# Optimization experiments

Measured on AMD Instinct MI355X. Metric: run time of the kernel, lower is better.

The kernel has to match this reference:

```python
import jax, jax.numpy as jnp
import numpy as np

B, Q, D, H, P, F = 16, 300, 256, 8, 4, 2048
HG = WG = 100          # feature-map height/width (hw = 10000, perfect square)
HW = HG * WG
DH = D // H
EPS = 1e-5


def _ln(x, g, b):
    m = x.mean(-1, keepdims=True)
    v = jnp.var(x, axis=-1, keepdims=True)
    return (x - m) * jax.lax.rsqrt(v + EPS) * g + b


def setup_inputs() -> dict:
    key = jax.random.key(0)
    ks = jax.random.split(key, 24)
    rn = lambda k, shape, s=0.02: jax.random.normal(k, shape, jnp.float32) * s
    return {
        "tgt": jax.random.normal(ks[0], (B, Q, D), jnp.float32),
        "memory": jax.random.normal(ks[1], (B, HW, D), jnp.float32),
        "in_proj_w": rn(ks[2], (D, 3 * D)), "in_proj_b": rn(ks[3], (3 * D,)),
        "out_proj_w": rn(ks[4], (D, D)), "out_proj_b": rn(ks[5], (D,)),
        "norm1_g": jnp.ones((D,), jnp.float32), "norm1_b": jnp.zeros((D,), jnp.float32),
        "ref_w": rn(ks[6], (D, 2)), "ref_b": rn(ks[7], (2,)),
        "off_w": rn(ks[8], (D, H * P * 2)), "off_b": rn(ks[9], (H * P * 2,)),
        "attw_w": rn(ks[10], (D, H * P)), "attw_b": rn(ks[11], (H * P,)),
        "vproj_w": rn(ks[12], (D, D)), "vproj_b": rn(ks[13], (D,)),
        "oproj_w": rn(ks[14], (D, D)), "oproj_b": rn(ks[15], (D,)),
        "norm2_g": jnp.ones((D,), jnp.float32), "norm2_b": jnp.zeros((D,), jnp.float32),
        "lin1_w": rn(ks[16], (D, F)), "lin1_b": rn(ks[17], (F,)),
        "lin2_w": rn(ks[18], (F, D)), "lin2_b": rn(ks[19], (D,)),
        "norm3_g": jnp.ones((D,), jnp.float32), "norm3_b": jnp.zeros((D,), jnp.float32),
    }


def reference(tgt, memory, in_proj_w, in_proj_b, out_proj_w, out_proj_b,
              norm1_g, norm1_b, ref_w, ref_b, off_w, off_b, attw_w, attw_b,
              vproj_w, vproj_b, oproj_w, oproj_b, norm2_g, norm2_b,
              lin1_w, lin1_b, lin2_w, lin2_b, norm3_g, norm3_b):
    # ---- self-attention (nn.MultiheadAttention, eval mode: dropout = identity)
    qkv = tgt @ in_proj_w + in_proj_b                      # [B,Q,3D]
    q, k, v = jnp.split(qkv, 3, axis=-1)
    q = q.reshape(B, Q, H, DH)
    k = k.reshape(B, Q, H, DH)
    v = v.reshape(B, Q, H, DH)
    scores = jnp.einsum('bqhd,bkhd->bhqk', q, k) / jnp.sqrt(jnp.float32(DH))
    attn = jax.nn.softmax(scores, axis=-1)
    sa = jnp.einsum('bhqk,bkhd->bqhd', attn, v).reshape(B, Q, D) @ out_proj_w + out_proj_b
    x = _ln(tgt + sa, norm1_g, norm1_b)

    # ---- reference points
    ref = jax.nn.sigmoid(x @ ref_w + ref_b)                # [B,Q,2] in (0,1)

    # ---- deformable cross-attention
    offs = (x @ off_w + off_b).reshape(B, Q, H, P, 2)
    wts = jax.nn.softmax((x @ attw_w + attw_b).reshape(B, Q, H, P), axis=-1)
    vals = (memory @ vproj_w + vproj_b).reshape(B, HW, H, DH)
    loc = jnp.clip(ref[:, :, None, None, :] + offs, 0.0, 1.0)
    sx = loc[..., 0] * (WG - 1)
    sy = loc[..., 1] * (HG - 1)
    x0 = jnp.floor(sx)
    y0 = jnp.floor(sy)
    x0i = jnp.clip(x0.astype(jnp.int32), 0, WG - 1)
    y0i = jnp.clip(y0.astype(jnp.int32), 0, HG - 1)
    x1i = jnp.clip(x0i + 1, 0, WG - 1)
    y1i = jnp.clip(y0i + 1, 0, HG - 1)
    wx1 = sx - x0
    wx0 = 1.0 - wx1
    wy1 = sy - y0
    wy0 = 1.0 - wy1
    bi = jnp.arange(B)[:, None, None, None]
    hi = jnp.arange(H)[None, None, :, None]

    def gather(yi, xi):                                    # [B,Q,H,P,DH]
        return vals[bi, yi * WG + xi, hi]

    samp = (gather(y0i, x0i) * (wx0 * wy0)[..., None]
            + gather(y1i, x0i) * (wx0 * wy1)[..., None]
            + gather(y0i, x1i) * (wx1 * wy0)[..., None]
            + gather(y1i, x1i) * (wx1 * wy1)[..., None])
    ca = (samp * wts[..., None]).sum(axis=3).reshape(B, Q, D) @ oproj_w + oproj_b
    x = _ln(x + ca, norm2_g, norm2_b)

    # ---- FFN
    ff = jax.nn.relu(x @ lin1_w + lin1_b) @ lin2_w + lin2_b
    return _ln(x + ff, norm3_g, norm3_b)
```

## Files before the change

### kernel.cpp

```cpp
#include <hip/hip_runtime.h>

#define NB   16
#define NQ   300
#define ND   256
#define NH   8
#define NP   4
#define NF   2048
#define NHW  10000
#define NWG  100
#define NROW 4800

typedef __attribute__((ext_vector_type(8))) short bf16x8;
typedef __attribute__((ext_vector_type(4))) float f32x4;

__device__ __forceinline__ unsigned short f2bf(float f) {
    unsigned u = __builtin_bit_cast(unsigned, f);
    u = (u + 0x7fffu + ((u >> 16) & 1u)) >> 16;
    return (unsigned short)u;
}
__device__ __forceinline__ float bf2f(unsigned short h) {
    unsigned u = ((unsigned)h) << 16;
    return __builtin_bit_cast(float, u);
}

__global__ __launch_bounds__(256) void transpose_cast(
    const float* __restrict__ w_in,  const float* __restrict__ w_out,
    const float* __restrict__ w_vp,  const float* __restrict__ w_op,
    const float* __restrict__ w_l1,  const float* __restrict__ w_l2,
    unsigned short* __restrict__ o_in, unsigned short* __restrict__ o_out,
    unsigned short* __restrict__ o_vp, unsigned short* __restrict__ o_op,
    unsigned short* __restrict__ o_l1, unsigned short* __restrict__ o_l2)
{
    __shared__ float ts[64][65];
    int b = blockIdx.x;
    const float* src; unsigned short* dst; int K, N, ncx;
    if      (b < 48)  { src = w_in;  dst = o_in;  K = 256;  N = 768;  ncx = 12; }
    else if (b < 64)  { src = w_out; dst = o_out; K = 256;  N = 256;  ncx = 4;  b -= 48; }
    else if (b < 80)  { src = w_vp;  dst = o_vp;  K = 256;  N = 256;  ncx = 4;  b -= 64; }
    else if (b < 96)  { src = w_op;  dst = o_op;  K = 256;  N = 256;  ncx = 4;  b -= 80; }
    else if (b < 224) { src = w_l1;  dst = o_l1;  K = 256;  N = 2048; ncx = 32; b -= 96; }
    else              { src = w_l2;  dst = o_l2;  K = 2048; N = 256;  ncx = 4;  b -= 224; }
    const int n0 = (b % ncx) * 64, k0 = (b / ncx) * 64;
    const int t = threadIdx.x;
    const int r = t >> 4, c = t & 15;
    #pragma unroll
    for (int j = 0; j < 4; j++) {
        float4 v = *(const float4*)(src + (long)(k0 + j * 16 + r) * N + n0 + c * 4);
        ts[j * 16 + r][c * 4 + 0] = v.x;
        ts[j * 16 + r][c * 4 + 1] = v.y;
        ts[j * 16 + r][c * 4 + 2] = v.z;
        ts[j * 16 + r][c * 4 + 3] = v.w;
    }
    __syncthreads();
    #pragma unroll
    for (int j = 0; j < 4; j++) {
        unsigned short o[4];
        #pragma unroll
        for (int i = 0; i < 4; i++)
            o[i] = f2bf(ts[c * 4 + i][j * 16 + r]);
        *(uint2*)(dst + (long)(n0 + j * 16 + r) * K + k0 + c * 4) = *(uint2*)o;
    }
}

__global__ __launch_bounds__(256) void prep_head(
    const float* __restrict__ rw, const float* __restrict__ rb,
    const float* __restrict__ ow, const float* __restrict__ ob,
    const float* __restrict__ aw, const float* __restrict__ ab,
    unsigned short* __restrict__ o_hd, float* __restrict__ o_hb)
{
    int id = blockIdx.x * 256 + threadIdx.x;
    if (id < 32768) {
        int n = id >> 8, k = id & 255;
        float v;
        if (n < 2)       v = rw[k * 2 + n];
        else if (n < 66) v = ow[k * 64 + (n - 2)];
        else if (n < 98) v = aw[k * 32 + (n - 66)];
        else             v = 0.0f;
        o_hd[id] = f2bf(v);
        return;
    }
    id -= 32768;
    if (id < 128) {
        float v;
        if (id < 2)       v = rb[id];
        else if (id < 66) v = ob[id - 2];
        else if (id < 98) v = ab[id - 66];
        else              v = 0.0f;
        o_hb[id] = v;
    }
}

template <int RELU, int OUTBF, int SPLITK, int TM>
__global__ __launch_bounds__(256, (TM == 64) ? 4 : 3) void gemm_bt(
    const float* __restrict__ A, const unsigned short* __restrict__ Bt,
    const float* __restrict__ bias, void* __restrict__ Cout,
    int M, int N, int K)
{
    constexpr int AI = TM / 32;
    constexpr int NI = TM / 32;
    __shared__ unsigned short As[2][TM][40];
    __shared__ unsigned short Bs[2][128][40];
    const int t    = threadIdx.x;
    const long m0  = (long)blockIdx.y * TM;
    const int  n0  = blockIdx.x * 128;
    const int  wave = t >> 6, lane = t & 63;
    const int  wm  = (wave >> 1) * (TM / 2);
    const int  wn  = (wave & 1) << 6;
    const int  l16 = lane & 15, quad = lane >> 4;
    const int  arow = t >> 3, acol = (t & 7) << 2;
    const int  brow = t >> 2, bcol = (t & 3) << 3;

    f32x4 acc[NI][4] = {};

    const int kChunk = K / SPLITK;
    const int kBeg   = (SPLITK > 1) ? blockIdx.z * kChunk : 0;
    const int nk     = kChunk / 32;

    float4 fa[AI];
    uint4  fb[2];

    auto loadAB = [&](int kt) {
        const int k0 = kBeg + kt * 32;
        #pragma unroll
        for (int j = 0; j < AI; j++) {
            const long r = m0 + j * 32 + arow;
            fa[j] = (r < M) ? *(const float4*)(A + r * (long)K + k0 + acol)
                            : make_float4(0.f, 0.f, 0.f, 0.f);
        }
        #pragma unroll
        for (int j = 0; j < 2; j++)
            fb[j] = *(const uint4*)(Bt + (long)(n0 + j * 64 + brow) * K + k0 + bcol);
    };
    auto storeLDS = [&](int buf) {
        #pragma unroll
        for (int j = 0; j < AI; j++) {
            unsigned short ta[4] = {f2bf(fa[j].x), f2bf(fa[j].y),
                                    f2bf(fa[j].z), f2bf(fa[j].w)};
            *(uint2*)&As[buf][j * 32 + arow][acol] = *(uint2*)ta;
        }
        #pragma unroll
        for (int j = 0; j < 2; j++)
            *(uint4*)&Bs[buf][j * 64 + brow][bcol] = fb[j];
    };

    loadAB(0);
    storeLDS(0);
    __syncthreads();

    for (int kt = 0; kt < nk; kt++) {
        const int cur = kt & 1;
        if (kt + 1 < nk) loadAB(kt + 1);

        bf16x8 af[NI], bfr[4];
        #pragma unroll
        for (int i = 0; i < NI; i++)
            af[i] = *(const bf16x8*)&As[cur][wm + i * 16 + l16][quad * 8];
        #pragma unroll
        for (int j = 0; j < 4; j++)
            bfr[j] = *(const bf16x8*)&Bs[cur][wn + j * 16 + l16][quad * 8];
        #pragma unroll
        for (int i = 0; i < NI; i++)
            #pragma unroll
            for (int j = 0; j < 4; j++)
                acc[i][j] = __builtin_amdgcn_mfma_f32_16x16x32_bf16(
                    bfr[j], af[i], acc[i][j], 0, 0, 0);

        if (kt + 1 < nk) {
            storeLDS(cur ^ 1);
            __syncthreads();
        }
    }

    float4 bj[4];
    #pragma unroll
    for (int j = 0; j < 4; j++)
        bj[j] = *(const float4*)&bias[n0 + wn + j * 16 + quad * 4];

    if (SPLITK > 1) {
        const float bscale = (blockIdx.z == 0) ? 1.0f : 0.0f;
        #pragma unroll
        for (int i = 0; i < NI; i++) {
            const long gr = m0 + wm + i * 16 + l16;
            if (gr < M) {
                #pragma unroll
                for (int j = 0; j < 4; j++) {
                    float* cp = (float*)Cout + gr * N + n0 + wn + j * 16 + quad * 4;
                    atomicAdd(cp + 0, acc[i][j][0] + bscale * bj[j].x);
                    atomicAdd(cp + 1, acc[i][j][1] + bscale * bj[j].y);
                    atomicAdd(cp + 2, acc[i][j][2] + bscale * bj[j].z);
                    atomicAdd(cp + 3, acc[i][j][3] + bscale * bj[j].w);
                }
            }
        }
        return;
    }

    #pragma unroll
    for (int i = 0; i < NI; i++) {
        const long gr = m0 + wm + i * 16 + l16;
        if (gr < M) {
            #pragma unroll
            for (int j = 0; j < 4; j++) {
                float4 v;
                v.x = acc[i][j][0] + bj[j].x;
                v.y = acc[i][j][1] + bj[j].y;
                v.z = acc[i][j][2] + bj[j].z;
                v.w = acc[i][j][3] + bj[j].w;
                if (RELU) {
                    v.x = fmaxf(v.x, 0.f); v.y = fmaxf(v.y, 0.f);
                    v.z = fmaxf(v.z, 0.f); v.w = fmaxf(v.w, 0.f);
                }
                const int gc = n0 + wn + j * 16 + quad * 4;
                if (OUTBF) {
                    unsigned short o[4] = {f2bf(v.x), f2bf(v.y), f2bf(v.z), f2bf(v.w)};
                    *(uint2*)((unsigned short*)Cout + gr * N + gc) = *(uint2*)o;
                } else {
                    *(float4*)((float*)Cout + gr * N + gc) = v;
                }
            }
        }
    }
}

__global__ __launch_bounds__(256) void attn_kernel(
    const float* __restrict__ qkv, float* __restrict__ sa)
{
    __shared__ union {
        struct {
            unsigned short Ks[304][40];
            unsigned short Qs[64][40];
        } s;
        unsigned short Ps[4][16][328];
    } u;
    __shared__ unsigned short Vt[32][328];

    const int bh = blockIdx.y;
    const int b  = bh >> 3, h = bh & 7;
    const int q0 = blockIdx.x * 64;
    const int t  = threadIdx.x;

    for (int idx = t; idx < 304 * 8; idx += 256) {
        const int r = idx >> 3, c4 = (idx & 7) << 2;
        if (r < NQ) {
            const float4 kv = *(const float4*)(qkv + ((long)(b * NQ + r)) * 768 + 256 + h * 32 + c4);
            u.s.Ks[r][c4 + 0] = f2bf(kv.x); u.s.Ks[r][c4 + 1] = f2bf(kv.y);
            u.s.Ks[r][c4 + 2] = f2bf(kv.z); u.s.Ks[r][c4 + 3] = f2bf(kv.w);
        } else {
            u.s.Ks[r][c4 + 0] = 0; u.s.Ks[r][c4 + 1] = 0;
            u.s.Ks[r][c4 + 2] = 0; u.s.Ks[r][c4 + 3] = 0;
        }
    }
    for (int idx = t; idx < NQ * 8; idx += 256) {
        const int key = idx >> 3, dq = (idx & 7) << 2;
        const float4 vv = *(const float4*)(qkv + ((long)(b * NQ + key)) * 768 + 512 + h * 32 + dq);
        Vt[dq + 0][key] = f2bf(vv.x); Vt[dq + 1][key] = f2bf(vv.y);
        Vt[dq + 2][key] = f2bf(vv.z); Vt[dq + 3][key] = f2bf(vv.w);
    }
    for (int idx = t; idx < 32 * 20; idx += 256)
        Vt[idx / 20][300 + idx % 20] = 0;
    for (int idx = t; idx < 64 * 8; idx += 256) {
        const int r = idx >> 3, c4 = (idx & 7) << 2;
        const int q = q0 + r;
        if (q < NQ) {
            const float4 qv = *(const float4*)(qkv + ((long)(b * NQ + q)) * 768 + h * 32 + c4);
            u.s.Qs[r][c4 + 0] = f2bf(qv.x); u.s.Qs[r][c4 + 1] = f2bf(qv.y);
            u.s.Qs[r][c4 + 2] = f2bf(qv.z); u.s.Qs[r][c4 + 3] = f2bf(qv.w);
        } else {
            u.s.Qs[r][c4 + 0] = 0; u.s.Qs[r][c4 + 1] = 0;
            u.s.Qs[r][c4 + 2] = 0; u.s.Qs[r][c4 + 3] = 0;
        }
    }
    __syncthreads();

    const int wave = t >> 6, lane = t & 63;
    const int l16 = lane & 15, quad = lane >> 4;
    const float scale = 0.1767766952966369f;

    const bf16x8 aq = *(const bf16x8*)&u.s.Qs[wave * 16 + l16][quad * 8];
    f32x4 sacc[19];
    #pragma unroll
    for (int kt = 0; kt < 19; kt++) {
        const bf16x8 bk = *(const bf16x8*)&u.s.Ks[kt * 16 + l16][quad * 8];
        sacc[kt] = __builtin_amdgcn_mfma_f32_16x16x32_bf16(
            aq, bk, (f32x4){0.f, 0.f, 0.f, 0.f}, 0, 0, 0);
    }

    float inv[4];
    #pragma unroll
    for (int r = 0; r < 4; r++) {
        float m = -1e30f;
        #pragma unroll
        for (int kt = 0; kt < 19; kt++) {
            float s = sacc[kt][r] * scale;
            if (kt == 18 && l16 >= 12) s = -1e30f;
            sacc[kt][r] = s;
            m = fmaxf(m, s);
        }
        m = fmaxf(m, __shfl_xor(m, 1)); m = fmaxf(m, __shfl_xor(m, 2));
        m = fmaxf(m, __shfl_xor(m, 4)); m = fmaxf(m, __shfl_xor(m, 8));
        float sum = 0.f;
        #pragma unroll
        for (int kt = 0; kt < 19; kt++) {
            float p = __expf(sacc[kt][r] - m);
            sacc[kt][r] = p;
            sum += p;
        }
        sum += __shfl_xor(sum, 1); sum += __shfl_xor(sum, 2);
        sum += __shfl_xor(sum, 4); sum += __shfl_xor(sum, 8);
        inv[r] = 1.0f / sum;
    }

    __syncthreads();

    #pragma unroll
    for (int kt = 0; kt < 19; kt++)
        #pragma unroll
        for (int r = 0; r < 4; r++)
            u.Ps[wave][quad * 4 + r][kt * 16 + l16] = f2bf(sacc[kt][r] * inv[r]);
    #pragma unroll
    for (int r = 0; r < 4; r++)
        u.Ps[wave][quad * 4 + r][304 + l16] = 0;

    f32x4 o0 = {0.f, 0.f, 0.f, 0.f}, o1 = {0.f, 0.f, 0.f, 0.f};
    #pragma unroll
    for (int kt = 0; kt < 10; kt++) {
        const bf16x8 ap  = *(const bf16x8*)&u.Ps[wave][l16][kt * 32 + quad * 8];
        const bf16x8 bv0 = *(const bf16x8*)&Vt[l16][kt * 32 + quad * 8];
        const bf16x8 bv1 = *(const bf16x8*)&Vt[16 + l16][kt * 32 + quad * 8];
        o0 = __builtin_amdgcn_mfma_f32_16x16x32_bf16(ap, bv0, o0, 0, 0, 0);
        o1 = __builtin_amdgcn_mfma_f32_16x16x32_bf16(ap, bv1, o1, 0, 0, 0);
    }

    #pragma unroll
    for (int r = 0; r < 4; r++) {
        const int q = q0 + wave * 16 + quad * 4 + r;
        if (q < NQ) {
            float* op = sa + ((long)(b * NQ + q)) * ND + h * 32;
            op[l16]      = o0[r];
            op[16 + l16] = o1[r];
        }
    }
}

__global__ __launch_bounds__(256) void residual_ln(
    const float* __restrict__ a, const float* __restrict__ r,
    const float* __restrict__ gam, const float* __restrict__ bet,
    float* __restrict__ out)
{
    const int row  = blockIdx.x * 4 + (threadIdx.x >> 6);
    const int lane = threadIdx.x & 63;
    const long base = (long)row * ND + lane * 4;
    float4 av = *(const float4*)(a + base);
    float4 rv = *(const float4*)(r + base);
    float x0 = av.x + rv.x, x1 = av.y + rv.y, x2 = av.z + rv.z, x3 = av.w + rv.w;
    float s  = x0 + x1 + x2 + x3;
    float s2 = x0 * x0 + x1 * x1 + x2 * x2 + x3 * x3;
    #pragma unroll
    for (int off = 32; off >= 1; off >>= 1) {
        s  += __shfl_xor(s, off);
        s2 += __shfl_xor(s2, off);
    }
    float mean = s * 0.00390625f;
    float var  = s2 * 0.00390625f - mean * mean;
    float rstd = rsqrtf(var + 1e-5f);
    float4 gv = *(const float4*)(gam + lane * 4);
    float4 bv = *(const float4*)(bet + lane * 4);
    float4 o;
    o.x = (x0 - mean) * rstd * gv.x + bv.x;
    o.y = (x1 - mean) * rstd * gv.y + bv.y;
    o.z = (x2 - mean) * rstd * gv.z + bv.z;
    o.w = (x3 - mean) * rstd * gv.w + bv.w;
    *(float4*)(out + base) = o;
}

__global__ __launch_bounds__(256) void meta_kernel(
    const float* __restrict__ res, float* __restrict__ meta)
{
    const int t   = threadIdx.x;
    const int row = blockIdx.x * 8 + (t >> 5);
    const int s   = t & 31;
    const int h   = s >> 2;
    const float* rp = res + (long)row * 128;
    const float rx = 1.f / (1.f + __expf(-rp[0]));
    const float ry = 1.f / (1.f + __expf(-rp[1]));
    const float offx = rp[2 + 2 * s], offy = rp[3 + 2 * s];
    const float a0 = rp[66 + h * 4 + 0], a1 = rp[66 + h * 4 + 1];
    const float a2 = rp[66 + h * 4 + 2], a3 = rp[66 + h * 4 + 3];
    const float mx = fmaxf(fmaxf(a0, a1), fmaxf(a2, a3));
    const float den = __expf(a0 - mx) + __expf(a1 - mx) +
                      __expf(a2 - mx) + __expf(a3 - mx);
    const float awt = __expf(rp[66 + s] - mx) / den;

    const float lx = fminf(fmaxf(rx + offx, 0.f), 1.f) * (NWG - 1);
    const float ly = fminf(fmaxf(ry + offy, 0.f), 1.f) * (NWG - 1);
    const float fx = floorf(lx), fy = floorf(ly);
    int x0 = (int)fx; x0 = min(max(x0, 0), NWG - 1);
    int y0 = (int)fy; y0 = min(max(y0, 0), NWG - 1);
    const int x1 = min(x0 + 1, NWG - 1);
    const int y1 = min(y0 + 1, NWG - 1);
    const float wx1 = lx - fx, wx0 = 1.f - wx1;
    const float wy1 = ly - fy, wy0 = 1.f - wy1;
    float4 m0, m1;
    m0.x = __int_as_float(y0 * NWG + x0);
    m0.y = __int_as_float(y0 * NWG + x1);
    m0.z = __int_as_float(y1 * NWG + x0);
    m0.w = __int_as_float(y1 * NWG + x1);
    m1.x = awt * wx0 * wy0;
    m1.y = awt * wx1 * wy0;
    m1.z = awt * wx0 * wy1;
    m1.w = awt * wx1 * wy1;
    float* mp = meta + (long)row * 256 + s * 8;
    *(float4*)mp       = m0;
    *(float4*)(mp + 4) = m1;
}

__global__ __launch_bounds__(256) void deform_gather(
    const float* __restrict__ meta, const unsigned short* __restrict__ vals,
    float* __restrict__ ca)
{
    const int row = blockIdx.x;
    const int b = row / NQ;
    __shared__ float ms[256];
    const int t = threadIdx.x;
    ms[t] = meta[(long)row * 256 + t];
    __syncthreads();
    const int h = t >> 5, d = t & 31;
    const unsigned short* vb = vals + (long)b * NHW * ND + h * 32 + d;
    float acc = 0.f;
    #pragma unroll
    for (int p = 0; p < NP; p++) {
        const float* mp = ms + h * 32 + p * 8;
        const int i00 = __float_as_int(mp[0]);
        const int i01 = __float_as_int(mp[1]);
        const int i10 = __float_as_int(mp[2]);
        const int i11 = __float_as_int(mp[3]);
        acc += mp[4] * bf2f(vb[(long)i00 * ND]);
        acc += mp[5] * bf2f(vb[(long)i01 * ND]);
        acc += mp[6] * bf2f(vb[(long)i10 * ND]);
        acc += mp[7] * bf2f(vb[(long)i11 * ND]);
    }
    ca[(long)row * ND + t] = acc;
}

extern "C" void kernel_launch(void* const* d_in, const int* in_sizes, int n_in,
                              void* d_out, int out_size, void* d_ws, size_t ws_size,
                              hipStream_t stream)
{
    (void)in_sizes; (void)n_in; (void)out_size; (void)ws_size;
    const float* tgt   = (const float*)d_in[0];
    const float* mem   = (const float*)d_in[1];
    const float* inpw  = (const float*)d_in[2];
    const float* inpb  = (const float*)d_in[3];
    const float* outw  = (const float*)d_in[4];
    const float* outb  = (const float*)d_in[5];
    const float* n1g   = (const float*)d_in[6];
    const float* n1b   = (const float*)d_in[7];
    const float* refw  = (const float*)d_in[8];
    const float* refb  = (const float*)d_in[9];
    const float* offw  = (const float*)d_in[10];
    const float* offb  = (const float*)d_in[11];
    const float* attww = (const float*)d_in[12];
    const float* attwb = (const float*)d_in[13];
    const float* vpw   = (const float*)d_in[14];
    const float* vpb   = (const float*)d_in[15];
    const float* opw   = (const float*)d_in[16];
    const float* opb   = (const float*)d_in[17];
    const float* n2g   = (const float*)d_in[18];
    const float* n2b   = (const float*)d_in[19];
    const float* l1w   = (const float*)d_in[20];
    const float* l1b   = (const float*)d_in[21];
    const float* l2w   = (const float*)d_in[22];
    const float* l2b   = (const float*)d_in[23];
    const float* n3g   = (const float*)d_in[24];
    const float* n3b   = (const float*)d_in[25];
    float* out = (float*)d_out;

    char* p = (char*)d_ws;
    auto alloc = [&](size_t bytes) {
        char* r = p; p += (bytes + 255) & ~(size_t)255; return (void*)r;
    };
    unsigned short* wtIn   = (unsigned short*)alloc(768 * 256 * 2);
    unsigned short* wtOut  = (unsigned short*)alloc(256 * 256 * 2);
    unsigned short* wtVp   = (unsigned short*)alloc(256 * 256 * 2);
    unsigned short* wtOp   = (unsigned short*)alloc(256 * 256 * 2);
    unsigned short* wtL1   = (unsigned short*)alloc(2048 * 256 * 2);
    unsigned short* wtL2   = (unsigned short*)alloc(256 * 2048 * 2);
    unsigned short* wtHead = (unsigned short*)alloc(128 * 256 * 2);
    float*          headb  = (float*)alloc(128 * 4);
    float* qkv  = (float*)alloc((size_t)NROW * 768 * 4);
    float* sa   = (float*)alloc((size_t)NROW * ND * 4);
    float* x1   = (float*)alloc((size_t)NROW * ND * 4);
    float* x2   = (float*)alloc((size_t)NROW * ND * 4);
    float* tmp  = (float*)alloc((size_t)NROW * ND * 4);
    float* ca   = (float*)alloc((size_t)NROW * ND * 4);
    float* meta = (float*)alloc((size_t)NROW * 256 * 4);
    void* uni = alloc((size_t)NB * NHW * ND * 2);
    unsigned short* vals = (unsigned short*)uni;
    float* h1 = (float*)uni;
    float* res = qkv;

    transpose_cast<<<352, 256, 0, stream>>>(
        inpw, outw, vpw, opw, l1w, l2w,
        wtIn, wtOut, wtVp, wtOp, wtL1, wtL2);
    prep_head<<<129, 256, 0, stream>>>(refw, refb, offw, offb, attww, attwb,
                                       wtHead, headb);

    gemm_bt<0, 0, 1, 64><<<dim3(6, 75), 256, 0, stream>>>(tgt, wtIn, inpb, qkv,
                                                          NROW, 768, 256);
    gemm_bt<0, 1, 1, 128><<<dim3(2, 1250), 256, 0, stream>>>(mem, wtVp, vpb, vals,
                                                             NB * NHW, 256, 256);
    attn_kernel<<<dim3(5, 128), 256, 0, stream>>>(qkv, sa);
    gemm_bt<0, 0, 1, 64><<<dim3(2, 75), 256, 0, stream>>>(sa, wtOut, outb, tmp,
                                                          NROW, 256, 256);
    residual_ln<<<1200, 256, 0, stream>>>(tgt, tmp, n1g, n1b, x1);
    gemm_bt<0, 0, 1, 64><<<dim3(1, 75), 256, 0, stream>>>(x1, wtHead, headb, res,
                                                          NROW, 128, 256);
    meta_kernel<<<600, 256, 0, stream>>>(res, meta);
    deform_gather<<<4800, 256, 0, stream>>>(meta, vals, ca);
    gemm_bt<0, 0, 1, 64><<<dim3(2, 75), 256, 0, stream>>>(ca, wtOp, opb, tmp,
                                                          NROW, 256, 256);
    residual_ln<<<1200, 256, 0, stream>>>(x1, tmp, n2g, n2b, x2);
    gemm_bt<1, 0, 1, 64><<<dim3(16, 75), 256, 0, stream>>>(x2, wtL1, l1b, h1,
                                                           NROW, 2048, 256);
    hipMemsetAsync(tmp, 0, (size_t)NROW * ND * 4, stream);
    gemm_bt<0, 0, 4, 64><<<dim3(2, 75, 4), 256, 0, stream>>>(h1, wtL2, l2b, tmp,
                                                             NROW, 256, 2048);
    residual_ln<<<1200, 256, 0, stream>>>(x2, tmp, n3g, n3b, out);
}
```

Baseline: 577.1 us.

## Add full-width vproj GEMM and replace split-K atomics with partial-sum buffers

Adds a dedicated value-projection GEMM in which each block computes a 128x256 output tile, so every A tile of the large memory tensor is loaded and converted to bf16 once instead of twice. The split-K FFN second GEMM now writes each K-slice to its own partial buffer instead of using atomicAdd, and the memset is dropped. The final residual LayerNorm sums the four partials before normalizing. The costs are extra workspace, larger accumulator register use (launch bound of 2 blocks per CU), and three more partial-tensor reads in the last LayerNorm.

After: 516.5 us. 1.12x faster.

```diff
diff --git a/kernel.cpp b/kernel.cpp
--- a/kernel.cpp
+++ b/kernel.cpp
@@ -87,6 +87,93 @@
         else if (id < 98) v = ab[id - 66];
         else              v = 0.0f;
         o_hb[id] = v;
+    }
+}
+
+__global__ __launch_bounds__(256, 2) void gemm_vproj(
+    const float* __restrict__ A, const unsigned short* __restrict__ Bt,
+    const float* __restrict__ bias, unsigned short* __restrict__ Cout)
+{
+    __shared__ unsigned short As[2][128][40];
+    __shared__ unsigned short Bs[2][256][40];
+    const int t    = threadIdx.x;
+    const long m0  = (long)blockIdx.x * 128;
+    const int  wave = t >> 6, lane = t & 63;
+    const int  wm  = (wave >> 1) << 6;
+    const int  wn  = (wave & 1) << 7;
+    const int  l16 = lane & 15, quad = lane >> 4;
+    const int  arow = t >> 3, acol = (t & 7) << 2;
+    const int  brow = t >> 2, bcol = (t & 3) << 3;
+
+    f32x4 acc[4][8] = {};
+    float4 fa[4];
+    uint4  fb[4];
+
+    auto loadAB = [&](int k0) {
+        #pragma unroll
+        for (int j = 0; j < 4; j++)
+            fa[j] = *(const float4*)(A + (m0 + j * 32 + arow) * 256L + k0 + acol);
+        #pragma unroll
+        for (int j = 0; j < 4; j++)
+            fb[j] = *(const uint4*)(Bt + (j * 64 + brow) * 256L + k0 + bcol);
+    };
+    auto storeLDS = [&](int buf) {
+        #pragma unroll
+        for (int j = 0; j < 4; j++) {
+            unsigned short ta[4] = {f2bf(fa[j].x), f2bf(fa[j].y),
+                                    f2bf(fa[j].z), f2bf(fa[j].w)};
+            *(uint2*)&As[buf][j * 32 + arow][acol] = *(uint2*)ta;
+        }
+        #pragma unroll
+        for (int j = 0; j < 4; j++)
+            *(uint4*)&Bs[buf][j * 64 + brow][bcol] = fb[j];
+    };
+
+    loadAB(0);
+    storeLDS(0);
+    __syncthreads();
+
+    for (int kt = 0; kt < 8; kt++) {
+        const int cur = kt & 1;
+        if (kt < 7) loadAB((kt + 1) * 32);
+
+        bf16x8 af[4], bfr[8];
+        #pragma unroll
+        for (int i = 0; i < 4; i++)
+            af[i] = *(const bf16x8*)&As[cur][wm + i * 16 + l16][quad * 8];
+        #pragma unroll
+        for (int j = 0; j < 8; j++)
+            bfr[j] = *(const bf16x8*)&Bs[cur][wn + j * 16 + l16][quad * 8];
+        #pragma unroll
+        for (int i = 0; i < 4; i++)
+            #pragma unroll
+            for (int j = 0; j < 8; j++)
+                acc[i][j] = __builtin_amdgcn_mfma_f32_16x16x32_bf16(
+                    bfr[j], af[i], acc[i][j], 0, 0, 0);
+
+        if (kt < 7) {
+            storeLDS(cur ^ 1);
+            __syncthreads();
+        }
+    }
+
+    float4 bj[8];
+    #pragma unroll
+    for (int j = 0; j < 8; j++)
+        bj[j] = *(const float4*)&bias[wn + j * 16 + quad * 4];
+
+    #pragma unroll
+    for (int i = 0; i < 4; i++) {
+        const long gr = m0 + wm + i * 16 + l16;
+        #pragma unroll
+        for (int j = 0; j < 8; j++) {
+            const int gc = wn + j * 16 + quad * 4;
+            unsigned short o[4] = {f2bf(acc[i][j][0] + bj[j].x),
+                                   f2bf(acc[i][j][1] + bj[j].y),
+                                   f2bf(acc[i][j][2] + bj[j].z),
+                                   f2bf(acc[i][j][3] + bj[j].w)};
+            *(uint2*)(Cout + gr * 256 + gc) = *(uint2*)o;
+        }
     }
 }
 
@@ -176,23 +263,11 @@
     for (int j = 0; j < 4; j++)
         bj[j] = *(const float4*)&bias[n0 + wn + j * 16 + quad * 4];
 
+    float* outp = (float*)Cout;
+    float bscale = 1.0f;
     if (SPLITK > 1) {
-        const float bscale = (blockIdx.z == 0) ? 1.0f : 0.0f;
-        #pragma unroll
-        for (int i = 0; i < NI; i++) {
-            const long gr = m0 + wm + i * 16 + l16;
-            if (gr < M) {
-                #pragma unroll
-                for (int j = 0; j < 4; j++) {
-                    float* cp = (float*)Cout + gr * N + n0 + wn + j * 16 + quad * 4;
-                    atomicAdd(cp + 0, acc[i][j][0] + bscale * bj[j].x);
-                    atomicAdd(cp + 1, acc[i][j][1] + bscale * bj[j].y);
-                    atomicAdd(cp + 2, acc[i][j][2] + bscale * bj[j].z);
-                    atomicAdd(cp + 3, acc[i][j][3] + bscale * bj[j].w);
-                }
-            }
-        }
-        return;
+        outp += (size_t)blockIdx.z * M * N;
+        bscale = (blockIdx.z == 0) ? 1.0f : 0.0f;
     }
 
     #pragma unroll
@@ -202,10 +277,10 @@
             #pragma unroll
             for (int j = 0; j < 4; j++) {
                 float4 v;
-                v.x = acc[i][j][0] + bj[j].x;
-                v.y = acc[i][j][1] + bj[j].y;
-                v.z = acc[i][j][2] + bj[j].z;
-                v.w = acc[i][j][3] + bj[j].w;
+                v.x = acc[i][j][0] + bscale * bj[j].x;
+                v.y = acc[i][j][1] + bscale * bj[j].y;
+                v.z = acc[i][j][2] + bscale * bj[j].z;
+                v.w = acc[i][j][3] + bscale * bj[j].w;
                 if (RELU) {
                     v.x = fmaxf(v.x, 0.f); v.y = fmaxf(v.y, 0.f);
                     v.z = fmaxf(v.z, 0.f); v.w = fmaxf(v.w, 0.f);
@@ -215,7 +290,7 @@
                     unsigned short o[4] = {f2bf(v.x), f2bf(v.y), f2bf(v.z), f2bf(v.w)};
                     *(uint2*)((unsigned short*)Cout + gr * N + gc) = *(uint2*)o;
                 } else {
-                    *(float4*)((float*)Cout + gr * N + gc) = v;
+                    *(float4*)(outp + gr * N + gc) = v;
                 }
             }
         }
@@ -342,16 +417,22 @@
     }
 }
 
+template <int NPART>
 __global__ __launch_bounds__(256) void residual_ln(
     const float* __restrict__ a, const float* __restrict__ r,
     const float* __restrict__ gam, const float* __restrict__ bet,
-    float* __restrict__ out)
+    float* __restrict__ out, long pstride)
 {
     const int row  = blockIdx.x * 4 + (threadIdx.x >> 6);
     const int lane = threadIdx.x & 63;
     const long base = (long)row * ND + lane * 4;
     float4 av = *(const float4*)(a + base);
     float4 rv = *(const float4*)(r + base);
+    #pragma unroll
+    for (int z = 1; z < NPART; z++) {
+        float4 pv = *(const float4*)(r + z * pstride + base);
+        rv.x += pv.x; rv.y += pv.y; rv.z += pv.z; rv.w += pv.w;
+    }
     float x0 = av.x + rv.x, x1 = av.y + rv.y, x2 = av.z + rv.z, x3 = av.w + rv.w;
     float s  = x0 + x1 + x2 + x3;
     float s2 = x0 * x0 + x1 * x1 + x2 * x2 + x3 * x3;
@@ -491,7 +572,7 @@
     float* sa   = (float*)alloc((size_t)NROW * ND * 4);
     float* x1   = (float*)alloc((size_t)NROW * ND * 4);
     float* x2   = (float*)alloc((size_t)NROW * ND * 4);
-    float* tmp  = (float*)alloc((size_t)NROW * ND * 4);
+    float* tmp  = (float*)alloc((size_t)NROW * ND * 4 * 4);
     float* ca   = (float*)alloc((size_t)NROW * ND * 4);
     float* meta = (float*)alloc((size_t)NROW * 256 * 4);
     void* uni = alloc((size_t)NB * NHW * ND * 2);
@@ -507,23 +588,22 @@
 
     gemm_bt<0, 0, 1, 64><<<dim3(6, 75), 256, 0, stream>>>(tgt, wtIn, inpb, qkv,
                                                           NROW, 768, 256);
-    gemm_bt<0, 1, 1, 128><<<dim3(2, 1250), 256, 0, stream>>>(mem, wtVp, vpb, vals,
-                                                             NB * NHW, 256, 256);
+    gemm_vproj<<<1250, 256, 0, stream>>>(mem, wtVp, vpb, vals);
     attn_kernel<<<dim3(5, 128), 256, 0, stream>>>(qkv, sa);
     gemm_bt<0, 0, 1, 64><<<dim3(2, 75), 256, 0, stream>>>(sa, wtOut, outb, tmp,
                                                           NROW, 256, 256);
-    residual_ln<<<1200, 256, 0, stream>>>(tgt, tmp, n1g, n1b, x1);
+    residual_ln<1><<<1200, 256, 0, stream>>>(tgt, tmp, n1g, n1b, x1, 0);
     gemm_bt<0, 0, 1, 64><<<dim3(1, 75), 256, 0, stream>>>(x1, wtHead, headb, res,
                                                           NROW, 128, 256);
     meta_kernel<<<600, 256, 0, stream>>>(res, meta);
     deform_gather<<<4800, 256, 0, stream>>>(meta, vals, ca);
     gemm_bt<0, 0, 1, 64><<<dim3(2, 75), 256, 0, stream>>>(ca, wtOp, opb, tmp,
                                                           NROW, 256, 256);
-    residual_ln<<<1200, 256, 0, stream>>>(x1, tmp, n2g, n2b, x2);
+    residual_ln<1><<<1200, 256, 0, stream>>>(x1, tmp, n2g, n2b, x2, 0);
     gemm_bt<1, 0, 1, 64><<<dim3(16, 75), 256, 0, stream>>>(x2, wtL1, l1b, h1,
                                                            NROW, 2048, 256);
-    hipMemsetAsync(tmp, 0, (size_t)NROW * ND * 4, stream);
     gemm_bt<0, 0, 4, 64><<<dim3(2, 75, 4), 256, 0, stream>>>(h1, wtL2, l2b, tmp,
                                                              NROW, 256, 2048);
-    residual_ln<<<1200, 256, 0, stream>>>(x2, tmp, n3g, n3b, out);
-}
+    residual_ln<4><<<1200, 256, 0, stream>>>(x2, tmp, n3g, n3b, out,
+                                             (long)NROW * ND);
+}
```
